# Optimization experiments

Measured on AMD Instinct MI355X. Metric: run time of the kernel, lower is better.

Reference implementation:

```python
import jax, jax.numpy as jnp
import numpy as np

B, N, C = 8, 4096, 512
H, DK, DV = 8, 64, 64


def _xnorm(x, gamma):
    # L2 norm over last dim, keepdim; scale by per-head gamma
    nrm = jnp.sqrt(jnp.sum(x * x, axis=-1, keepdims=True))
    return x * gamma / nrm


def setup_inputs() -> dict:
    key = jax.random.key(0)
    ks = jax.random.split(key, 9)
    inp = {
        "queries": jax.random.normal(ks[0], (B, N, C), dtype=jnp.float32),
        "keys": jax.random.normal(ks[1], (B, N, C), dtype=jnp.float32),
        "values": jax.random.normal(ks[2], (B, N, C), dtype=jnp.float32),
        # Linear weights stored torch-style [out, in]; init.normal_(std=0.001), bias=0
        "Wq": jax.random.normal(ks[3], (H * DK, C), dtype=jnp.float32) * 0.001,
        "bq": jnp.zeros((H * DK,), dtype=jnp.float32),
        "Wk": jax.random.normal(ks[4], (H * DK, C), dtype=jnp.float32) * 0.001,
        "bk": jnp.zeros((H * DK,), dtype=jnp.float32),
        "Wv": jax.random.normal(ks[5], (H * DV, C), dtype=jnp.float32) * 0.001,
        "bv": jnp.zeros((H * DV,), dtype=jnp.float32),
        "Wo": jax.random.normal(ks[6], (C, H * DV), dtype=jnp.float32) * 0.001,
        "bo": jnp.zeros((C,), dtype=jnp.float32),
        "gamma": jax.random.normal(ks[7], (1, H, 1, 1), dtype=jnp.float32),
    }
    return inp


def reference(queries, keys, values, Wq, bq, Wk, bk, Wv, bv, Wo, bo, gamma):
    bs, nq, _ = queries.shape
    nk = keys.shape[1]
    # projections -> [b, h, n, d]
    q = (queries @ Wq.T + bq).reshape(bs, nq, H, DK).transpose(0, 2, 1, 3)
    k = (keys @ Wk.T + bk).reshape(bs, nk, H, DK).transpose(0, 2, 1, 3)
    v = (values @ Wv.T + bv).reshape(bs, nk, H, DV).transpose(0, 2, 1, 3)
    # kv: [b, h, dk, dv]  (small intermediate)
    kv = jnp.einsum('bhnk,bhnv->bhkv', k, v)
    kv_n = _xnorm(kv, gamma)     # norm over dv
    q_n = _xnorm(q, gamma)       # norm over dk
    out = jnp.einsum('bhnk,bhkv->bhnv', q_n, kv_n)  # [b,h,nq,dv]
    out = out.transpose(0, 2, 1, 3).reshape(bs, nq, H * DV)
    return out @ Wo.T + bo
```

## Files before the change

kernel.cpp:

```cpp
#include <hip/hip_runtime.h>


typedef __attribute__((ext_vector_type(4))) float f32x4;
typedef __attribute__((ext_vector_type(8))) short s16x8;
typedef __attribute__((ext_vector_type(4))) unsigned short u16x4;
typedef __attribute__((ext_vector_type(8))) unsigned short u16x8;

#define DEVFN __device__ __forceinline__

DEVFN unsigned short f2b(float f) {
  union { float f; unsigned u; } un; un.f = f;
  unsigned r = un.u + 0x7fffu + ((un.u >> 16) & 1u);
  return (unsigned short)(r >> 16);
}
DEVFN float b2f(unsigned short us) {
  union { unsigned u; float f; } un; un.u = ((unsigned)us) << 16;
  return un.f;
}

DEVFN void gl_lds16(const void* g, void* l) {
  __builtin_amdgcn_global_load_lds(
      (const __attribute__((address_space(1))) unsigned*)g,
      (__attribute__((address_space(3))) unsigned*)l, 16, 0, 0);
}

template <bool AF32, typename CT>
DEVFN void gemm_core(const void* Ain, const unsigned short* Bt,
                     const float* bias, CT* C, bool qnorm, const float* gamma,
                     int bx, int by) {
  constexpr int KK = 512, NN = 512;
  __shared__ unsigned short As[128 * 64];
  __shared__ unsigned short Bs[2][128 * 64];
  const int tid = threadIdx.x, lane = tid & 63, wid = tid >> 6;
  const int wm = (wid >> 1) * 64, wn = (wid & 1) * 64;
  const int r = lane & 15, g = lane >> 4;

  const float* Af = nullptr;
  const unsigned short* Ab = nullptr;
  if constexpr (AF32)
    Af = (const float*)Ain + (long)(bx * 128 + (tid >> 4)) * KK + (tid & 15) * 4;
  else
    Ab = (const unsigned short*)Ain + (long)(bx * 128 + (tid >> 3)) * KK + (tid & 7) * 8;

  const char* Bsrc = (const char*)Bt +
                     ((long)(by * 128 + wid * 32 + (lane >> 3)) * (KK * 2)) +
                     (((lane & 7) ^ (lane >> 3)) * 16);

  f32x4 PAf[8];
  u16x8 PAb[4];
  f32x4 acc[4][4] = {};

#define ISSUE_A(KT)                                                            \
  {                                                                            \
    if constexpr (AF32) {                                                      \
      _Pragma("unroll") for (int i = 0; i < 8; ++i)                            \
          PAf[i] = *reinterpret_cast<const f32x4*>(                            \
              Af + (long)i * 16 * KK + (KT)*64);                               \
    } else {                                                                   \
      _Pragma("unroll") for (int i = 0; i < 4; ++i)                            \
          PAb[i] = *reinterpret_cast<const u16x8*>(                            \
              Ab + (long)i * 32 * KK + (KT)*64);                               \
    }                                                                          \
  }

#define STAGE_B(BUF, KT)                                                       \
  {                                                                            \
    _Pragma("unroll") for (int q = 0; q < 4; ++q)                              \
        gl_lds16(Bsrc + q * 8192 + (KT)*128,                                   \
                 (char*)Bs[BUF] + wid * 4096 + q * 1024);                      \
  }

#define WRITE_A                                                                \
  {                                                                            \
    if constexpr (AF32) {                                                      \
      const int rr = tid >> 4, cb = (tid & 15) * 8;                            \
      _Pragma("unroll") for (int i = 0; i < 8; ++i) {                          \
        int row = i * 16 + rr;                                                 \
        int off = row * 128 + (cb ^ ((row & 7) << 4));                         \
        u16x4 o = {f2b(PAf[i][0]), f2b(PAf[i][1]),                             \
                   f2b(PAf[i][2]), f2b(PAf[i][3])};                            \
        *reinterpret_cast<u16x4*>(reinterpret_cast<char*>(As) + off) = o;      \
      }                                                                        \
    } else {                                                                   \
      const int rr = tid >> 3, cb = (tid & 7) * 16;                            \
      _Pragma("unroll") for (int i = 0; i < 4; ++i) {                          \
        int row = i * 32 + rr;                                                 \
        int off = row * 128 + (cb ^ ((row & 7) << 4));                         \
        *reinterpret_cast<u16x8*>(reinterpret_cast<char*>(As) + off) = PAb[i]; \
      }                                                                        \
    }                                                                          \
  }

#define COMPUTE(BBUF)                                                          \
  {                                                                            \
    _Pragma("unroll") for (int ks = 0; ks < 2; ++ks) {                         \
      s16x8 a[4], b[4];                                                        \
      const int kb = ks * 64 + g * 16;                                         \
      _Pragma("unroll") for (int i = 0; i < 4; ++i) {                          \
        int ar = wm + i * 16 + r;                                              \
        a[i] = *reinterpret_cast<const s16x8*>(                                \
            reinterpret_cast<const char*>(As) + ar * 128 +                     \
            (kb ^ ((ar & 7) << 4)));                                           \
        int br = wn + i * 16 + r;                                              \
        b[i] = *reinterpret_cast<const s16x8*>(                                \
            reinterpret_cast<const char*>(Bs[BBUF]) + br * 128 +               \
            (kb ^ ((br & 7) << 4)));                                           \
      }                                                                        \
      _Pragma("unroll") for (int i = 0; i < 4; ++i)                            \
          _Pragma("unroll") for (int j = 0; j < 4; ++j) acc[i][j] =            \
          __builtin_amdgcn_mfma_f32_16x16x32_bf16(a[i], b[j], acc[i][j], 0,    \
                                                  0, 0);                       \
    }                                                                          \
  }

#define SB0 __builtin_amdgcn_sched_barrier(0);
#define BAR_RAW                                                                \
  SB0 __builtin_amdgcn_s_barrier(); SB0
#define END_BAR                                                                \
  asm volatile("s_waitcnt vmcnt(0) lgkmcnt(0)" ::: "memory");                  \
  SB0 __builtin_amdgcn_s_barrier(); SB0

  ISSUE_A(0)
  STAGE_B(0, 0)
  WRITE_A
  END_BAR
  ISSUE_A(1) STAGE_B(1, 1) SB0 COMPUTE(0) BAR_RAW WRITE_A END_BAR
  ISSUE_A(2) STAGE_B(0, 2) SB0 COMPUTE(1) BAR_RAW WRITE_A END_BAR
  ISSUE_A(3) STAGE_B(1, 3) SB0 COMPUTE(0) BAR_RAW WRITE_A END_BAR
  ISSUE_A(4) STAGE_B(0, 4) SB0 COMPUTE(1) BAR_RAW WRITE_A END_BAR
  ISSUE_A(5) STAGE_B(1, 5) SB0 COMPUTE(0) BAR_RAW WRITE_A END_BAR
  ISSUE_A(6) STAGE_B(0, 6) SB0 COMPUTE(1) BAR_RAW WRITE_A END_BAR
  ISSUE_A(7) STAGE_B(1, 7) SB0 COMPUTE(0) BAR_RAW WRITE_A END_BAR
  COMPUTE(1)

#undef ISSUE_A
#undef STAGE_B
#undef WRITE_A
#undef COMPUTE
#undef BAR_RAW
#undef END_BAR
#undef SB0

  const int crow0 = bx * 128 + wm + g * 4;
  const int ccol0 = by * 128 + wn + r;
#pragma unroll
  for (int j = 0; j < 4; ++j) {
    float bv = bias[ccol0 + j * 16];
#pragma unroll
    for (int i = 0; i < 4; ++i)
#pragma unroll
      for (int ii = 0; ii < 4; ++ii) acc[i][j][ii] += bv;
  }
  if (qnorm) {
    const int h = (by * 128 + wn) >> 6;
    const float gam = gamma[h];
#pragma unroll
    for (int i = 0; i < 4; ++i)
#pragma unroll
      for (int ii = 0; ii < 4; ++ii) {
        float s = 0.f;
#pragma unroll
        for (int j = 0; j < 4; ++j) s += acc[i][j][ii] * acc[i][j][ii];
        s += __shfl_xor(s, 1);
        s += __shfl_xor(s, 2);
        s += __shfl_xor(s, 4);
        s += __shfl_xor(s, 8);
        float sc = gam / sqrtf(s);
#pragma unroll
        for (int j = 0; j < 4; ++j) acc[i][j][ii] *= sc;
      }
  }
#pragma unroll
  for (int i = 0; i < 4; ++i)
#pragma unroll
    for (int j = 0; j < 4; ++j)
#pragma unroll
      for (int ii = 0; ii < 4; ++ii) {
        long row = crow0 + i * 16 + ii;
        int col = ccol0 + j * 16;
        if constexpr (sizeof(CT) == 2)
          C[row * NN + col] = f2b(acc[i][j][ii]);
        else
          C[row * NN + col] = acc[i][j][ii];
      }
}

DEVFN void swz_xy(int bid, int nwg, int& bx, int& by) {
  int s = (bid & 7) * (nwg >> 3) + (bid >> 3);
  bx = s >> 2;
  by = s & 3;
}

__global__ __launch_bounds__(256, 3)
void proj_qkv(const float* __restrict__ Aq, const float* __restrict__ Ak,
              const float* __restrict__ Av, const unsigned short* __restrict__ Bq,
              const unsigned short* __restrict__ Bk, const unsigned short* __restrict__ Bv,
              const float* __restrict__ bq, const float* __restrict__ bk,
              const float* __restrict__ bv, unsigned short* __restrict__ Cq,
              unsigned short* __restrict__ Ck, unsigned short* __restrict__ Cv,
              const float* __restrict__ gamma) {
  const int z = blockIdx.z;
  const float* A = z == 0 ? Aq : (z == 1 ? Ak : Av);
  const unsigned short* B = z == 0 ? Bq : (z == 1 ? Bk : Bv);
  const float* bias = z == 0 ? bq : (z == 1 ? bk : bv);
  unsigned short* C = z == 0 ? Cq : (z == 1 ? Ck : Cv);
  int bx, by;
  swz_xy(blockIdx.x, 1024, bx, by);
  gemm_core<true, unsigned short>(A, B, bias, C, z == 0, gamma, bx, by);
}

__global__ __launch_bounds__(256, 3)
void gemm_final(const unsigned short* __restrict__ q, const unsigned short* __restrict__ Mt,
                const float* __restrict__ bo, float* __restrict__ out) {
  const int zb = blockIdx.z;
  int bx, by;
  swz_xy(blockIdx.x, 128, bx, by);
  gemm_core<false, float>(q + (long)zb * 2097152, Mt + (long)zb * 262144, bo,
                          out + (long)zb * 2097152, false, nullptr, bx, by);
}

#define NCHUNK 16
__global__ __launch_bounds__(256, 2)
void kv_partial(const unsigned short* __restrict__ kq,
                const unsigned short* __restrict__ vq,
                float* __restrict__ part) {
  const int tid = threadIdx.x;
  const int chunk = blockIdx.x;
  const int bh = blockIdx.y;
  const int b = bh >> 3, h = bh & 7;
  __shared__ float ks[32][64];
  __shared__ float vs[32][64];
  const int dk0 = (tid & 15) * 4;
  const int dv0 = (tid >> 4) * 4;
  float acc[4][4] = {};
  const long nbase = (long)b * 4096 + chunk * 256;

  for (int sub = 0; sub < 8; ++sub) {
    long n0 = nbase + sub * 32;
#pragma unroll
    for (int i = 0; i < 2; ++i) {
      int e = i * 256 + tid;
      int row = e >> 4, c4 = e & 15;
      long gofs = (n0 + row) * 512 + h * 64 + c4 * 4;
      u16x4 kk = *reinterpret_cast<const u16x4*>(kq + gofs);
      u16x4 vv = *reinterpret_cast<const u16x4*>(vq + gofs);
      f32x4 kf = {b2f(kk[0]), b2f(kk[1]), b2f(kk[2]), b2f(kk[3])};
      f32x4 vf = {b2f(vv[0]), b2f(vv[1]), b2f(vv[2]), b2f(vv[3])};
      *reinterpret_cast<f32x4*>(&ks[row][c4 * 4]) = kf;
      *reinterpret_cast<f32x4*>(&vs[row][c4 * 4]) = vf;
    }
    __syncthreads();
#pragma unroll 4
    for (int n = 0; n < 32; ++n) {
      f32x4 kk = *reinterpret_cast<const f32x4*>(&ks[n][dk0]);
      f32x4 vv = *reinterpret_cast<const f32x4*>(&vs[n][dv0]);
#pragma unroll
      for (int a = 0; a < 4; ++a)
#pragma unroll
        for (int c = 0; c < 4; ++c)
          acc[a][c] += kk[a] * vv[c];
    }
    __syncthreads();
  }
  float* pg = part + ((long)chunk * 64 + bh) * 4096;
#pragma unroll
  for (int a = 0; a < 4; ++a) {
    f32x4 o = {acc[a][0], acc[a][1], acc[a][2], acc[a][3]};
    *reinterpret_cast<f32x4*>(pg + (dk0 + a) * 64 + dv0) = o;
  }
}

__global__ __launch_bounds__(256)
void kv_normN(const float* __restrict__ part, const float* __restrict__ gamma,
              unsigned short* __restrict__ kvn) {
  const int bh = blockIdx.x, h = bh & 7;
  const int tid = threadIdx.x;
  __shared__ float kvs[4096];
  __shared__ float scale[64];
#pragma unroll
  for (int i = 0; i < 4; ++i) {
    int e4 = i * 256 + tid;
    const float* p = part + (long)bh * 4096 + e4 * 4;
    f32x4 s = {0.f, 0.f, 0.f, 0.f};
#pragma unroll
    for (int c = 0; c < NCHUNK; ++c) {
      f32x4 v = *reinterpret_cast<const f32x4*>(p + (long)c * 64 * 4096);
      s += v;
    }
    *reinterpret_cast<f32x4*>(kvs + e4 * 4) = s;
  }
  __syncthreads();
  if (tid < 64) {
    float s = 0.f;
    for (int dv = 0; dv < 64; ++dv) { float x = kvs[tid * 64 + dv]; s += x * x; }
    scale[tid] = gamma[h] / sqrtf(s);
  }
  __syncthreads();
#pragma unroll
  for (int i = 0; i < 4; ++i) {
    int e4 = i * 256 + tid;
    float sc = scale[e4 >> 4];
    f32x4 v = *reinterpret_cast<const f32x4*>(kvs + e4 * 4);
    u16x4 o = {f2b(v[0] * sc), f2b(v[1] * sc), f2b(v[2] * sc), f2b(v[3] * sc)};
    *reinterpret_cast<u16x4*>(kvn + (long)bh * 4096 + e4 * 4) = o;
  }
}

__global__ __launch_bounds__(64)
void mt_kernel(const unsigned short* __restrict__ Wo_b,
               const unsigned short* __restrict__ kvn,
               unsigned short* __restrict__ Mt) {
  const int bid = blockIdx.x;
  const int bh = bid >> 2, seg = bid & 3;
  const int b = bh >> 3, h = bh & 7;
  const int lane = threadIdx.x;
  const int r = lane & 15, g = lane >> 4;
  f32x4 acc[8][4] = {};
  s16x8 bf[2][4];
#pragma unroll
  for (int ks = 0; ks < 2; ++ks)
#pragma unroll
    for (int j = 0; j < 4; ++j)
      bf[ks][j] = *reinterpret_cast<const s16x8*>(
          kvn + (long)bh * 4096 + (j * 16 + r) * 64 + ks * 32 + g * 8);
#pragma unroll
  for (int ks = 0; ks < 2; ++ks)
#pragma unroll
    for (int i = 0; i < 8; ++i) {
      s16x8 af = *reinterpret_cast<const s16x8*>(
          Wo_b + (long)(seg * 128 + i * 16 + r) * 512 + h * 64 + ks * 32 + g * 8);
#pragma unroll
      for (int j = 0; j < 4; ++j)
        acc[i][j] = __builtin_amdgcn_mfma_f32_16x16x32_bf16(af, bf[ks][j], acc[i][j], 0, 0, 0);
    }
#pragma unroll
  for (int i = 0; i < 8; ++i)
#pragma unroll
    for (int j = 0; j < 4; ++j)
#pragma unroll
      for (int ii = 0; ii < 4; ++ii) {
        int c = seg * 128 + i * 16 + g * 4 + ii;
        int dk = j * 16 + r;
        Mt[(long)b * 262144 + (long)c * 512 + h * 64 + dk] = f2b(acc[i][j][ii]);
      }
}

__global__ void cast4(const float* __restrict__ a0, const float* __restrict__ a1,
                      const float* __restrict__ a2, const float* __restrict__ a3,
                      unsigned short* __restrict__ o0, unsigned short* __restrict__ o1,
                      unsigned short* __restrict__ o2, unsigned short* __restrict__ o3) {
  const int y = blockIdx.y;
  const float* in = y == 0 ? a0 : (y == 1 ? a1 : (y == 2 ? a2 : a3));
  unsigned short* out = y == 0 ? o0 : (y == 1 ? o1 : (y == 2 ? o2 : o3));
  int i = blockIdx.x * 256 + threadIdx.x;
  f32x4 v = reinterpret_cast<const f32x4*>(in)[i];
  reinterpret_cast<u16x4*>(out)[i] = u16x4{f2b(v[0]), f2b(v[1]), f2b(v[2]), f2b(v[3])};
}

extern "C" void kernel_launch(void* const* d_in, const int* in_sizes, int n_in,
                              void* d_out, int out_size, void* d_ws, size_t ws_size,
                              hipStream_t stream) {
  const float* queries = (const float*)d_in[0];
  const float* keys    = (const float*)d_in[1];
  const float* values  = (const float*)d_in[2];
  const float* Wq = (const float*)d_in[3];
  const float* bq = (const float*)d_in[4];
  const float* Wk = (const float*)d_in[5];
  const float* bk = (const float*)d_in[6];
  const float* Wv = (const float*)d_in[7];
  const float* bv = (const float*)d_in[8];
  const float* Wo = (const float*)d_in[9];
  const float* bo = (const float*)d_in[10];
  const float* gamma = (const float*)d_in[11];

  unsigned short* Wq_b = (unsigned short*)d_ws;
  unsigned short* Wk_b = Wq_b + 262144;
  unsigned short* Wv_b = Wk_b + 262144;
  unsigned short* Wo_b = Wv_b + 262144;
  unsigned short* q_b  = Wo_b + 262144;
  unsigned short* kvn  = q_b + 16777216;
  float* part = (float*)(kvn + 262144);
  unsigned short* Mt = (unsigned short*)part;
  unsigned short* k_b = (unsigned short*)d_out;
  unsigned short* v_b = k_b + 16777216;
  float* out = (float*)d_out;

  cast4<<<dim3(256, 4), 256, 0, stream>>>(Wq, Wk, Wv, Wo, Wq_b, Wk_b, Wv_b, Wo_b);

  proj_qkv<<<dim3(1024, 1, 3), 256, 0, stream>>>(
      queries, keys, values, Wq_b, Wk_b, Wv_b, bq, bk, bv, q_b, k_b, v_b, gamma);

  kv_partial<<<dim3(NCHUNK, 64), 256, 0, stream>>>(k_b, v_b, part);
  kv_normN<<<64, 256, 0, stream>>>(part, gamma, kvn);
  mt_kernel<<<256, 64, 0, stream>>>(Wo_b, kvn, Mt);

  gemm_final<<<dim3(128, 1, 8), 256, 0, stream>>>(q_b, Mt, bo, out);
}
```

Before: 185.8 us.

## Stage A tiles via direct global-to-LDS loads and convert fp32 at fragment load

A tiles are now loaded straight into LDS with global_load_lds, as B already was, instead of going through registers with an fp32-to-bf16 conversion before the LDS write. For fp32 inputs the raw floats are stored with an XOR swizzle and converted to bf16 when each MFMA fragment is read. The B double buffer and the hand-scheduled overlapping barriers are dropped in favour of a single buffer with plain __syncthreads around each stage. This removes register staging and VGPR pressure, but serialises load and compute and doubles the LDS bytes per A tile in the fp32 case.

```diff
diff --git a/kernel.cpp b/kernel.cpp
--- a/kernel.cpp
+++ b/kernel.cpp
@@ -29,82 +29,72 @@
                      const float* bias, CT* C, bool qnorm, const float* gamma,
                      int bx, int by) {
   constexpr int KK = 512, NN = 512;
-  __shared__ unsigned short As[128 * 64];
-  __shared__ unsigned short Bs[2][128 * 64];
+  __shared__ __align__(16) char AsLDS[AF32 ? 32768 : 16384];
+  __shared__ __align__(16) char BsLDS[16384];
   const int tid = threadIdx.x, lane = tid & 63, wid = tid >> 6;
   const int wm = (wid >> 1) * 64, wn = (wid & 1) * 64;
   const int r = lane & 15, g = lane >> 4;
 
-  const float* Af = nullptr;
-  const unsigned short* Ab = nullptr;
-  if constexpr (AF32)
-    Af = (const float*)Ain + (long)(bx * 128 + (tid >> 4)) * KK + (tid & 15) * 4;
-  else
-    Ab = (const unsigned short*)Ain + (long)(bx * 128 + (tid >> 3)) * KK + (tid & 7) * 8;
-
   const char* Bsrc = (const char*)Bt +
-                     ((long)(by * 128 + wid * 32 + (lane >> 3)) * (KK * 2)) +
-                     (((lane & 7) ^ (lane >> 3)) * 16);
-
-  f32x4 PAf[8];
-  u16x8 PAb[4];
+      (long)(by * 128 + wid * 32 + (lane >> 3)) * 1024 +
+      (((lane & 7) ^ (lane >> 3)) * 16);
+  const char* Asrc_e = nullptr;
+  const char* Asrc_o = nullptr;
+  if constexpr (AF32) {
+    const char* ab = (const char*)Ain +
+        (long)(bx * 128 + wid * 32 + (lane >> 4)) * 2048;
+    Asrc_e = ab + (((lane & 15) ^ (lane >> 4)) * 16);
+    Asrc_o = ab + (((lane & 15) ^ (4 + (lane >> 4))) * 16);
+  } else {
+    Asrc_e = (const char*)Ain +
+        (long)(bx * 128 + wid * 32 + (lane >> 3)) * 1024 +
+        (((lane & 7) ^ (lane >> 3)) * 16);
+  }
+
   f32x4 acc[4][4] = {};
 
-#define ISSUE_A(KT)                                                            \
+#define STAGE(KT)                                                              \
   {                                                                            \
     if constexpr (AF32) {                                                      \
-      _Pragma("unroll") for (int i = 0; i < 8; ++i)                            \
-          PAf[i] = *reinterpret_cast<const f32x4*>(                            \
-              Af + (long)i * 16 * KK + (KT)*64);                               \
+      _Pragma("unroll") for (int q = 0; q < 8; ++q)                            \
+          gl_lds16((q & 1 ? Asrc_o : Asrc_e) + q * 8192 + (KT)*256,            \
+                   AsLDS + (wid * 8 + q) * 1024);                              \
     } else {                                                                   \
-      _Pragma("unroll") for (int i = 0; i < 4; ++i)                            \
-          PAb[i] = *reinterpret_cast<const u16x8*>(                            \
-              Ab + (long)i * 32 * KK + (KT)*64);                               \
+      _Pragma("unroll") for (int q = 0; q < 4; ++q)                            \
+          gl_lds16(Asrc_e + q * 8192 + (KT)*128,                               \
+                   AsLDS + wid * 4096 + q * 1024);                             \
     }                                                                          \
-  }
-
-#define STAGE_B(BUF, KT)                                                       \
-  {                                                                            \
     _Pragma("unroll") for (int q = 0; q < 4; ++q)                              \
         gl_lds16(Bsrc + q * 8192 + (KT)*128,                                   \
-                 (char*)Bs[BUF] + wid * 4096 + q * 1024);                      \
-  }
-
-#define WRITE_A                                                                \
-  {                                                                            \
-    if constexpr (AF32) {                                                      \
-      const int rr = tid >> 4, cb = (tid & 15) * 8;                            \
-      _Pragma("unroll") for (int i = 0; i < 8; ++i) {                          \
-        int row = i * 16 + rr;                                                 \
-        int off = row * 128 + (cb ^ ((row & 7) << 4));                         \
-        u16x4 o = {f2b(PAf[i][0]), f2b(PAf[i][1]),                             \
-                   f2b(PAf[i][2]), f2b(PAf[i][3])};                            \
-        *reinterpret_cast<u16x4*>(reinterpret_cast<char*>(As) + off) = o;      \
-      }                                                                        \
-    } else {                                                                   \
-      const int rr = tid >> 3, cb = (tid & 7) * 16;                            \
-      _Pragma("unroll") for (int i = 0; i < 4; ++i) {                          \
-        int row = i * 32 + rr;                                                 \
-        int off = row * 128 + (cb ^ ((row & 7) << 4));                         \
-        *reinterpret_cast<u16x8*>(reinterpret_cast<char*>(As) + off) = PAb[i]; \
-      }                                                                        \
-    }                                                                          \
-  }
-
-#define COMPUTE(BBUF)                                                          \
+                 BsLDS + wid * 4096 + q * 1024);                               \
+  }
+
+#define COMPUTE                                                                \
   {                                                                            \
     _Pragma("unroll") for (int ks = 0; ks < 2; ++ks) {                         \
       s16x8 a[4], b[4];                                                        \
       const int kb = ks * 64 + g * 16;                                         \
       _Pragma("unroll") for (int i = 0; i < 4; ++i) {                          \
         int ar = wm + i * 16 + r;                                              \
-        a[i] = *reinterpret_cast<const s16x8*>(                                \
-            reinterpret_cast<const char*>(As) + ar * 128 +                     \
-            (kb ^ ((ar & 7) << 4)));                                           \
+        if constexpr (AF32) {                                                  \
+          const int kc = ks * 128 + g * 32;                                    \
+          f32x4 alo = *reinterpret_cast<const f32x4*>(                         \
+              AsLDS + ar * 256 + (kc ^ ((ar & 7) << 4)));                      \
+          f32x4 ahi = *reinterpret_cast<const f32x4*>(                         \
+              AsLDS + ar * 256 + ((kc + 16) ^ ((ar & 7) << 4)));               \
+          s16x8 av;                                                            \
+          av[0] = (short)f2b(alo[0]); av[1] = (short)f2b(alo[1]);              \
+          av[2] = (short)f2b(alo[2]); av[3] = (short)f2b(alo[3]);              \
+          av[4] = (short)f2b(ahi[0]); av[5] = (short)f2b(ahi[1]);              \
+          av[6] = (short)f2b(ahi[2]); av[7] = (short)f2b(ahi[3]);              \
+          a[i] = av;                                                           \
+        } else {                                                               \
+          a[i] = *reinterpret_cast<const s16x8*>(                              \
+              AsLDS + ar * 128 + (kb ^ ((ar & 7) << 4)));                      \
+        }                                                                      \
         int br = wn + i * 16 + r;                                              \
         b[i] = *reinterpret_cast<const s16x8*>(                                \
-            reinterpret_cast<const char*>(Bs[BBUF]) + br * 128 +               \
-            (kb ^ ((br & 7) << 4)));                                           \
+            BsLDS + br * 128 + (kb ^ ((br & 7) << 4)));                        \
       }                                                                        \
       _Pragma("unroll") for (int i = 0; i < 4; ++i)                            \
           _Pragma("unroll") for (int j = 0; j < 4; ++j) acc[i][j] =            \
@@ -113,33 +103,21 @@
     }                                                                          \
   }
 
-#define SB0 __builtin_amdgcn_sched_barrier(0);
-#define BAR_RAW                                                                \
-  SB0 __builtin_amdgcn_s_barrier(); SB0
-#define END_BAR                                                                \
-  asm volatile("s_waitcnt vmcnt(0) lgkmcnt(0)" ::: "memory");                  \
-  SB0 __builtin_amdgcn_s_barrier(); SB0
-
-  ISSUE_A(0)
-  STAGE_B(0, 0)
-  WRITE_A
-  END_BAR
-  ISSUE_A(1) STAGE_B(1, 1) SB0 COMPUTE(0) BAR_RAW WRITE_A END_BAR
-  ISSUE_A(2) STAGE_B(0, 2) SB0 COMPUTE(1) BAR_RAW WRITE_A END_BAR
-  ISSUE_A(3) STAGE_B(1, 3) SB0 COMPUTE(0) BAR_RAW WRITE_A END_BAR
-  ISSUE_A(4) STAGE_B(0, 4) SB0 COMPUTE(1) BAR_RAW WRITE_A END_BAR
-  ISSUE_A(5) STAGE_B(1, 5) SB0 COMPUTE(0) BAR_RAW WRITE_A END_BAR
-  ISSUE_A(6) STAGE_B(0, 6) SB0 COMPUTE(1) BAR_RAW WRITE_A END_BAR
-  ISSUE_A(7) STAGE_B(1, 7) SB0 COMPUTE(0) BAR_RAW WRITE_A END_BAR
-  COMPUTE(1)
-
-#undef ISSUE_A
-#undef STAGE_B
-#undef WRITE_A
+#define SYNC __syncthreads();
+
+  STAGE(0) SYNC
+  COMPUTE SYNC STAGE(1) SYNC
+  COMPUTE SYNC STAGE(2) SYNC
+  COMPUTE SYNC STAGE(3) SYNC
+  COMPUTE SYNC STAGE(4) SYNC
+  COMPUTE SYNC STAGE(5) SYNC
+  COMPUTE SYNC STAGE(6) SYNC
+  COMPUTE SYNC STAGE(7) SYNC
+  COMPUTE
+
+#undef STAGE
 #undef COMPUTE
-#undef BAR_RAW
-#undef END_BAR
-#undef SB0
+#undef SYNC
 
   const int crow0 = bx * 128 + wm + g * 4;
   const int ccol0 = by * 128 + wn + r;
```

Measured after the change: 192.8 us. 1.04x slower.
